# Kernel tuning notes

Measured on AMD Instinct MI355X. Metric: run time of the kernel, lower is better.

## Reference

```python
import jax, jax.numpy as jnp
import numpy as np

N_NODES = 100000
N_EDGES = 3200000
IN_FEATS = 512
HIDDEN = 16
NUM_CLASSES = 40


def setup_inputs() -> dict:
    key = jax.random.key(0)
    k1, k2, k3, k4, k5, k6 = jax.random.split(key, 6)
    x = jax.random.normal(k1, (N_NODES, IN_FEATS), dtype=jnp.float32)
    edge_index = jax.random.randint(k2, (2, N_EDGES), 0, N_NODES, dtype=jnp.int64)
    # Glorot-ish init for GCN weights
    W1 = jax.random.normal(k3, (IN_FEATS, HIDDEN), dtype=jnp.float32) / np.sqrt(IN_FEATS)
    b1 = jnp.zeros((HIDDEN,), dtype=jnp.float32)
    W2 = jax.random.normal(k4, (HIDDEN, NUM_CLASSES), dtype=jnp.float32) / np.sqrt(HIDDEN)
    b2 = jnp.zeros((NUM_CLASSES,), dtype=jnp.float32)
    return {"x": x, "edge_index": edge_index, "W1": W1, "b1": b1, "W2": W2, "b2": b2}


def _gcn_norm(edge_index, num_nodes):
    # Add self-loops (PyG GCNConv default), then symmetric normalization
    loops = jnp.arange(num_nodes, dtype=edge_index.dtype)
    src = jnp.concatenate([edge_index[0], loops])
    dst = jnp.concatenate([edge_index[1], loops])
    deg = jax.ops.segment_sum(jnp.ones_like(dst, dtype=jnp.float32), dst,
                              num_segments=num_nodes)
    dinv = jnp.where(deg > 0, jax.lax.rsqrt(deg), 0.0)
    norm = dinv[src] * dinv[dst]  # [E + N]
    return src, dst, norm


def _gcn_conv(x, W, b, src, dst, norm, num_nodes):
    h = x @ W                                   # transform first: [N, d_out]
    msg = h[src] * norm[:, None]                # gather + scale: [E+N, d_out]
    agg = jax.ops.segment_sum(msg, dst, num_segments=num_nodes)
    return agg + b


def reference(x, edge_index, W1, b1, W2, b2):
    num_nodes = x.shape[0]
    src, dst, norm = _gcn_norm(edge_index, num_nodes)
    h = _gcn_conv(x, W1, b1, src, dst, norm, num_nodes)
    h = jax.nn.relu(h)
    # F.dropout(training=self.training): eval mode -> identity (deterministic reference)
    h = _gcn_conv(h, W2, b2, src, dst, norm, num_nodes)
    return jax.nn.log_softmax(h, axis=1)
```

## Files before the change

### kernel.cpp

```cpp
#include <hip/hip_runtime.h>
#include <hip/hip_bf16.h>
#include <math.h>

#define N_NODES 100000
#define N_EDGES 3200000
#define IN_F    512
#define HID     16
#define NCLS    40
#define NB      2048
#define NPB     49
#define CAPW    2048
#define NBLK    256
#define EPB     12500

typedef unsigned short ushort_t;

__device__ __forceinline__ float bf16_to_f32(ushort_t u) {
    unsigned int b = ((unsigned int)u) << 16;
    return __uint_as_float(b);
}
__device__ __forceinline__ ushort_t f32_to_bf16(float f) {
    __hip_bfloat16 h = __float2bfloat16(f);
    return *(ushort_t*)&h;
}

__device__ __forceinline__ int load_edge(const void* ei, int is64, int idx) {
    if (is64) return (int)((const long long*)ei)[idx];
    return ((const int*)ei)[idx];
}

__global__ __launch_bounds__(256) void kPre(const int* __restrict__ ei,
                                            int* __restrict__ flag,
                                            int* __restrict__ gcur) {
    int i = blockIdx.x * 256 + threadIdx.x;
    if (i < NB) gcur[i] = i * CAPW;
    if (blockIdx.x == 0) {
        __shared__ int s_nz;
        if (threadIdx.x == 0) s_nz = 0;
        __syncthreads();
        int nz = 0;
        for (int k = threadIdx.x; k < 1024; k += 256)
            if (ei[2 * k + 1] != 0) nz = 1;
        if (nz) atomicOr(&s_nz, 1);
        __syncthreads();
        if (threadIdx.x == 0) flag[0] = s_nz ? 0 : 1;
    }
}

__global__ __launch_bounds__(256) void kB(const void* __restrict__ ei,
                                          const int* __restrict__ flag,
                                          int* __restrict__ gcur,
                                          int* __restrict__ binned) {
    __shared__ int hist[NB];
    __shared__ int base[NB];
    for (int i = threadIdx.x; i < NB; i += 256) hist[i] = 0;
    __syncthreads();
    int is64 = flag[0];
    int off0 = blockIdx.x * EPB;
    for (int i = threadIdx.x; i < EPB; i += 256) {
        int d = load_edge(ei, is64, N_EDGES + off0 + i);
        atomicAdd(&hist[d / NPB], 1);
    }
    __syncthreads();
    for (int i = threadIdx.x; i < NB; i += 256) {
        int c = hist[i];
        base[i] = c ? atomicAdd(&gcur[i], c) : 0;
        hist[i] = 0;
    }
    __syncthreads();
    for (int i = threadIdx.x; i < EPB; i += 256) {
        int s = load_edge(ei, is64, off0 + i);
        int d = load_edge(ei, is64, N_EDGES + off0 + i);
        int b = d / NPB;
        int o = atomicAdd(&hist[b], 1);
        binned[base[b] + o] = (s << 6) | (d - b * NPB);
    }
}

__global__ __launch_bounds__(256) void kSort(const int* __restrict__ gcur,
                                             int* __restrict__ binned,
                                             int* __restrict__ nstart,
                                             int* __restrict__ bend,
                                             float* __restrict__ dinv) {
    __shared__ int elist[CAPW];
    __shared__ int ih[NPB];
    __shared__ int lscan[NPB + 1];
    int b = blockIdx.x, tid = threadIdx.x;
    int beg = b * CAPW;
    int cnt = gcur[b] - beg;
    if (cnt > CAPW) cnt = CAPW;
    if (cnt < 0) cnt = 0;
    if (tid < NPB) ih[tid] = 0;
    __syncthreads();
    for (int k = tid; k < cnt; k += 256) {
        int p = binned[beg + k];
        elist[k] = p;
        atomicAdd(&ih[p & 63], 1);
    }
    __syncthreads();
    if (tid == 0) {
        int run = 0;
        for (int i = 0; i < NPB; ++i) { lscan[i] = run; run += ih[i]; }
        lscan[NPB] = run;
        bend[b] = beg + run;
    }
    __syncthreads();
    if (tid < NPB) {
        int n = b * NPB + tid;
        if (n < N_NODES) dinv[n] = rsqrtf((float)(ih[tid] + 1));
        nstart[n] = beg + lscan[tid];
        ih[tid] = lscan[tid];
    }
    __syncthreads();
    for (int k = tid; k < cnt; k += 256) {
        int p = elist[k];
        int pos = atomicAdd(&ih[p & 63], 1);
        binned[beg + pos] = p >> 6;
    }
}

__global__ __launch_bounds__(128) void k_gemm1(const float* __restrict__ x,
                                               const float* __restrict__ W1,
                                               const float* __restrict__ dinv,
                                               ushort_t* __restrict__ hsb) {
    __shared__ float Ws[IN_F * HID];
    for (int i = threadIdx.x; i < IN_F * HID; i += 128) Ws[i] = W1[i];
    __syncthreads();
    int n = blockIdx.x * 128 + threadIdx.x;
    if (n >= N_NODES) return;
    float acc[HID];
#pragma unroll
    for (int j = 0; j < HID; ++j) acc[j] = 0.0f;
    const float4* xr = (const float4*)(x + (size_t)n * IN_F);
    for (int k4 = 0; k4 < IN_F / 4; ++k4) {
        float4 xv = xr[k4];
        int kb = k4 * 4;
#pragma unroll
        for (int i = 0; i < 4; ++i) {
            float xs = (&xv.x)[i];
            const float4* wr = (const float4*)(Ws + (kb + i) * HID);
#pragma unroll
            for (int j4 = 0; j4 < 4; ++j4) {
                float4 w = wr[j4];
                acc[j4 * 4 + 0] += xs * w.x;
                acc[j4 * 4 + 1] += xs * w.y;
                acc[j4 * 4 + 2] += xs * w.z;
                acc[j4 * 4 + 3] += xs * w.w;
            }
        }
    }
    float di = dinv[n];
    ushort_t* hn = hsb + (size_t)n * HID;
#pragma unroll
    for (int j = 0; j < HID; ++j) hn[j] = f32_to_bf16(acc[j] * di);
}

__global__ __launch_bounds__(256) void kAgg1(const int* __restrict__ nstart,
                                             const int* __restrict__ bend,
                                             const int* __restrict__ sorted,
                                             const ushort_t* __restrict__ hsb,
                                             const float* __restrict__ dinv,
                                             const float* __restrict__ b1,
                                             ushort_t* __restrict__ h1sb) {
    int tid = threadIdx.x;
    int g = tid >> 4, lane = tid & 15;
    int n = blockIdx.x * 16 + g;
    int b = n / NPB, il = n - b * NPB;
    int beg = nstart[n];
    int end = (il == NPB - 1) ? bend[b] : nstart[n + 1];
    float acc = 0.0f;
    int k = beg;
    for (; k + 4 <= end; k += 4) {
        int s0 = sorted[k + 0], s1 = sorted[k + 1];
        int s2 = sorted[k + 2], s3 = sorted[k + 3];
        float v0 = bf16_to_f32(hsb[(size_t)s0 * HID + lane]);
        float v1 = bf16_to_f32(hsb[(size_t)s1 * HID + lane]);
        float v2 = bf16_to_f32(hsb[(size_t)s2 * HID + lane]);
        float v3 = bf16_to_f32(hsb[(size_t)s3 * HID + lane]);
        acc += (v0 + v1) + (v2 + v3);
    }
    for (; k < end; ++k)
        acc += bf16_to_f32(hsb[(size_t)sorted[k] * HID + lane]);
    float di = dinv[n];
    float self = bf16_to_f32(hsb[(size_t)n * HID + lane]);
    float v = di * (acc + self) + b1[lane];
    h1sb[(size_t)n * HID + lane] = f32_to_bf16(fmaxf(v, 0.0f) * di);
}

__global__ __launch_bounds__(256) void kAggOut(const int* __restrict__ nstart,
                                               const int* __restrict__ bend,
                                               const int* __restrict__ sorted,
                                               const ushort_t* __restrict__ h1sb,
                                               const float* __restrict__ dinv,
                                               const float* __restrict__ W2,
                                               const float* __restrict__ b2,
                                               float* __restrict__ out) {
    __shared__ float a2[16][HID + 1];
    __shared__ float Ws[HID * NCLS];
    __shared__ float bs[NCLS];
    int tid = threadIdx.x;
    for (int i = tid; i < HID * NCLS; i += 256) Ws[i] = W2[i];
    for (int i = tid; i < NCLS; i += 256) bs[i] = b2[i];

    int g = tid >> 4, lane = tid & 15;
    int n = blockIdx.x * 16 + g;
    int b = n / NPB, il = n - b * NPB;
    int beg = nstart[n];
    int end = (il == NPB - 1) ? bend[b] : nstart[n + 1];
    float acc = 0.0f;
    int k = beg;
    for (; k + 4 <= end; k += 4) {
        int s0 = sorted[k + 0], s1 = sorted[k + 1];
        int s2 = sorted[k + 2], s3 = sorted[k + 3];
        float v0 = bf16_to_f32(h1sb[(size_t)s0 * HID + lane]);
        float v1 = bf16_to_f32(h1sb[(size_t)s1 * HID + lane]);
        float v2 = bf16_to_f32(h1sb[(size_t)s2 * HID + lane]);
        float v3 = bf16_to_f32(h1sb[(size_t)s3 * HID + lane]);
        acc += (v0 + v1) + (v2 + v3);
    }
    for (; k < end; ++k)
        acc += bf16_to_f32(h1sb[(size_t)sorted[k] * HID + lane]);
    float di = dinv[n];
    float self = bf16_to_f32(h1sb[(size_t)n * HID + lane]);
    a2[g][lane] = di * (acc + self);
    __syncthreads();

    int v = g;
    int cidx = lane;
    float av[HID];
#pragma unroll
    for (int j = 0; j < HID; ++j) av[j] = a2[v][j];
    float l0 = bs[cidx], l1 = bs[cidx + 16];
    float l2 = (cidx < 8) ? bs[cidx + 32] : -1e30f;
#pragma unroll
    for (int j = 0; j < HID; ++j) {
        const float* wr = Ws + j * NCLS;
        l0 += av[j] * wr[cidx];
        l1 += av[j] * wr[cidx + 16];
        if (cidx < 8) l2 += av[j] * wr[cidx + 32];
    }
    float m = fmaxf(l0, fmaxf(l1, l2));
#pragma unroll
    for (int off = 8; off >= 1; off >>= 1)
        m = fmaxf(m, __shfl_xor(m, off, 16));
    float e = expf(l0 - m) + expf(l1 - m) + ((cidx < 8) ? expf(l2 - m) : 0.0f);
#pragma unroll
    for (int off = 8; off >= 1; off >>= 1)
        e += __shfl_xor(e, off, 16);
    float lse = m + logf(e);
    int nn = blockIdx.x * 16 + v;
    float* on = out + (size_t)nn * NCLS;
    on[cidx] = l0 - lse;
    on[cidx + 16] = l1 - lse;
    if (cidx < 8) on[cidx + 32] = l2 - lse;
}

extern "C" void kernel_launch(void* const* d_in, const int* in_sizes, int n_in,
                              void* d_out, int out_size, void* d_ws, size_t ws_size,
                              hipStream_t stream) {
    const float* x  = (const float*)d_in[0];
    const void*  ei = d_in[1];
    const float* W1 = (const float*)d_in[2];
    const float* b1 = (const float*)d_in[3];
    const float* W2 = (const float*)d_in[4];
    const float* b2 = (const float*)d_in[5];
    float* out = (float*)d_out;

    int*      iws    = (int*)d_ws;
    float*    fws    = (float*)d_ws;
    int*      gcur   = iws;
    int*      bend   = iws + 2048;
    int*      flag   = iws + 4096;
    float*    dinv   = fws + 8192;
    int*      nstart = iws + 108192;
    ushort_t* hsb    = (ushort_t*)(iws + 212992);
    ushort_t* h1sb   = (ushort_t*)(iws + 1012992);
    int*      binned = iws + 1812992;

    const int B = 256;

    kPre<<<(NB + B - 1) / B, B, 0, stream>>>((const int*)ei, flag, gcur);
    kB<<<NBLK, B, 0, stream>>>(ei, flag, gcur, binned);
    kSort<<<NB, B, 0, stream>>>(gcur, binned, nstart, bend, dinv);
    k_gemm1<<<(N_NODES + 127) / 128, 128, 0, stream>>>(x, W1, dinv, hsb);
    kAgg1<<<N_NODES / 16, B, 0, stream>>>(nstart, bend, binned, hsb, dinv, b1, h1sb);
    kAggOut<<<N_NODES / 16, B, 0, stream>>>(nstart, bend, binned, h1sb, dinv, W2, b2, out);
}
```

Measured before the change: 239.3 us.

## Run GEMM1 concurrently with edge binning in one kernel, defer dinv scaling

Merges the dense x@W1 projection and the edge-binning pass into one launch, with blocks split by index between the two roles, so the bandwidth-heavy GEMM overlaps with the atomic-heavy binning. Because dinv is not known yet when the GEMM runs, the GEMM writes unscaled bf16 rows and kSort rescales them by dinv after computing degrees. This adds a second bf16 rounding and an extra read-modify-write of hsb. GEMM blocks now use 256 threads instead of 128, with the same 32 KB of shared memory per block.

```diff
diff --git a/kernel.cpp b/kernel.cpp
--- a/kernel.cpp
+++ b/kernel.cpp
@@ -12,6 +12,7 @@
 #define CAPW    2048
 #define NBLK    256
 #define EPB     12500
+#define GEMM_BLKS 391
 
 typedef unsigned short ushort_t;
 
@@ -47,33 +48,70 @@
     }
 }
 
-__global__ __launch_bounds__(256) void kB(const void* __restrict__ ei,
-                                          const int* __restrict__ flag,
-                                          int* __restrict__ gcur,
-                                          int* __restrict__ binned) {
-    __shared__ int hist[NB];
-    __shared__ int base[NB];
-    for (int i = threadIdx.x; i < NB; i += 256) hist[i] = 0;
-    __syncthreads();
-    int is64 = flag[0];
-    int off0 = blockIdx.x * EPB;
-    for (int i = threadIdx.x; i < EPB; i += 256) {
-        int d = load_edge(ei, is64, N_EDGES + off0 + i);
-        atomicAdd(&hist[d / NPB], 1);
-    }
-    __syncthreads();
-    for (int i = threadIdx.x; i < NB; i += 256) {
-        int c = hist[i];
-        base[i] = c ? atomicAdd(&gcur[i], c) : 0;
-        hist[i] = 0;
-    }
-    __syncthreads();
-    for (int i = threadIdx.x; i < EPB; i += 256) {
-        int s = load_edge(ei, is64, off0 + i);
-        int d = load_edge(ei, is64, N_EDGES + off0 + i);
-        int b = d / NPB;
-        int o = atomicAdd(&hist[b], 1);
-        binned[base[b] + o] = (s << 6) | (d - b * NPB);
+__global__ __launch_bounds__(256) void kMega(const float* __restrict__ x,
+                                             const float* __restrict__ W1,
+                                             ushort_t* __restrict__ hsb,
+                                             const void* __restrict__ ei,
+                                             const int* __restrict__ flag,
+                                             int* __restrict__ gcur,
+                                             int* __restrict__ binned) {
+    __shared__ __align__(16) char smraw[IN_F * HID * 4];
+    int tid = threadIdx.x;
+    if (blockIdx.x < GEMM_BLKS) {
+        float* Ws = (float*)smraw;
+        for (int i = tid; i < IN_F * HID; i += 256) Ws[i] = W1[i];
+        __syncthreads();
+        int n = blockIdx.x * 256 + tid;
+        if (n >= N_NODES) return;
+        float acc[HID];
+#pragma unroll
+        for (int j = 0; j < HID; ++j) acc[j] = 0.0f;
+        const float4* xr = (const float4*)(x + (size_t)n * IN_F);
+        for (int k4 = 0; k4 < IN_F / 4; ++k4) {
+            float4 xv = xr[k4];
+            int kb = k4 * 4;
+#pragma unroll
+            for (int i = 0; i < 4; ++i) {
+                float xs = (&xv.x)[i];
+                const float4* wr = (const float4*)(Ws + (kb + i) * HID);
+#pragma unroll
+                for (int j4 = 0; j4 < 4; ++j4) {
+                    float4 w = wr[j4];
+                    acc[j4 * 4 + 0] += xs * w.x;
+                    acc[j4 * 4 + 1] += xs * w.y;
+                    acc[j4 * 4 + 2] += xs * w.z;
+                    acc[j4 * 4 + 3] += xs * w.w;
+                }
+            }
+        }
+        ushort_t* hn = hsb + (size_t)n * HID;
+#pragma unroll
+        for (int j = 0; j < HID; ++j) hn[j] = f32_to_bf16(acc[j]);
+    } else {
+        int* hist = (int*)smraw;
+        int* base = (int*)(smraw + NB * 4);
+        for (int i = tid; i < NB; i += 256) hist[i] = 0;
+        __syncthreads();
+        int is64 = flag[0];
+        int off0 = (blockIdx.x - GEMM_BLKS) * EPB;
+        for (int i = tid; i < EPB; i += 256) {
+            int d = load_edge(ei, is64, N_EDGES + off0 + i);
+            atomicAdd(&hist[d / NPB], 1);
+        }
+        __syncthreads();
+        for (int i = tid; i < NB; i += 256) {
+            int c = hist[i];
+            base[i] = c ? atomicAdd(&gcur[i], c) : 0;
+            hist[i] = 0;
+        }
+        __syncthreads();
+        for (int i = tid; i < EPB; i += 256) {
+            int s = load_edge(ei, is64, off0 + i);
+            int d = load_edge(ei, is64, N_EDGES + off0 + i);
+            int b = d / NPB;
+            int o = atomicAdd(&hist[b], 1);
+            binned[base[b] + o] = (s << 6) | (d - b * NPB);
+        }
     }
 }
 
@@ -81,10 +119,12 @@
                                              int* __restrict__ binned,
                                              int* __restrict__ nstart,
                                              int* __restrict__ bend,
-                                             float* __restrict__ dinv) {
+                                             float* __restrict__ dinv,
+                                             ushort_t* __restrict__ hsb) {
     __shared__ int elist[CAPW];
     __shared__ int ih[NPB];
     __shared__ int lscan[NPB + 1];
+    __shared__ float sdinv[NPB];
     int b = blockIdx.x, tid = threadIdx.x;
     int beg = b * CAPW;
     int cnt = gcur[b] - beg;
@@ -107,7 +147,9 @@
     __syncthreads();
     if (tid < NPB) {
         int n = b * NPB + tid;
-        if (n < N_NODES) dinv[n] = rsqrtf((float)(ih[tid] + 1));
+        float di = rsqrtf((float)(ih[tid] + 1));
+        sdinv[tid] = di;
+        if (n < N_NODES) dinv[n] = di;
         nstart[n] = beg + lscan[tid];
         ih[tid] = lscan[tid];
     }
@@ -117,42 +159,14 @@
         int pos = atomicAdd(&ih[p & 63], 1);
         binned[beg + pos] = p >> 6;
     }
-}
-
-__global__ __launch_bounds__(128) void k_gemm1(const float* __restrict__ x,
-                                               const float* __restrict__ W1,
-                                               const float* __restrict__ dinv,
-                                               ushort_t* __restrict__ hsb) {
-    __shared__ float Ws[IN_F * HID];
-    for (int i = threadIdx.x; i < IN_F * HID; i += 128) Ws[i] = W1[i];
-    __syncthreads();
-    int n = blockIdx.x * 128 + threadIdx.x;
-    if (n >= N_NODES) return;
-    float acc[HID];
-#pragma unroll
-    for (int j = 0; j < HID; ++j) acc[j] = 0.0f;
-    const float4* xr = (const float4*)(x + (size_t)n * IN_F);
-    for (int k4 = 0; k4 < IN_F / 4; ++k4) {
-        float4 xv = xr[k4];
-        int kb = k4 * 4;
-#pragma unroll
-        for (int i = 0; i < 4; ++i) {
-            float xs = (&xv.x)[i];
-            const float4* wr = (const float4*)(Ws + (kb + i) * HID);
-#pragma unroll
-            for (int j4 = 0; j4 < 4; ++j4) {
-                float4 w = wr[j4];
-                acc[j4 * 4 + 0] += xs * w.x;
-                acc[j4 * 4 + 1] += xs * w.y;
-                acc[j4 * 4 + 2] += xs * w.z;
-                acc[j4 * 4 + 3] += xs * w.w;
-            }
-        }
-    }
-    float di = dinv[n];
-    ushort_t* hn = hsb + (size_t)n * HID;
-#pragma unroll
-    for (int j = 0; j < HID; ++j) hn[j] = f32_to_bf16(acc[j] * di);
+    for (int u = tid; u < NPB * HID; u += 256) {
+        int i = u >> 4, j = u & 15;
+        int n = b * NPB + i;
+        if (n < N_NODES) {
+            size_t idx = (size_t)n * HID + j;
+            hsb[idx] = f32_to_bf16(bf16_to_f32(hsb[idx]) * sdinv[i]);
+        }
+    }
 }
 
 __global__ __launch_bounds__(256) void kAgg1(const int* __restrict__ nstart,
@@ -225,8 +239,7 @@
     a2[g][lane] = di * (acc + self);
     __syncthreads();
 
-    int v = g;
-    int cidx = lane;
+    int v = g, cidx = lane;
     float av[HID];
 #pragma unroll
     for (int j = 0; j < HID; ++j) av[j] = a2[v][j];
@@ -280,9 +293,8 @@
     const int B = 256;
 
     kPre<<<(NB + B - 1) / B, B, 0, stream>>>((const int*)ei, flag, gcur);
-    kB<<<NBLK, B, 0, stream>>>(ei, flag, gcur, binned);
-    kSort<<<NB, B, 0, stream>>>(gcur, binned, nstart, bend, dinv);
-    k_gemm1<<<(N_NODES + 127) / 128, 128, 0, stream>>>(x, W1, dinv, hsb);
+    kMega<<<GEMM_BLKS + NBLK, B, 0, stream>>>(x, W1, hsb, ei, flag, gcur, binned);
+    kSort<<<NB, B, 0, stream>>>(gcur, binned, nstart, bend, dinv, hsb);
     kAgg1<<<N_NODES / 16, B, 0, stream>>>(nstart, bend, binned, hsb, dinv, b1, h1sb);
     kAggOut<<<N_NODES / 16, B, 0, stream>>>(nstart, bend, binned, h1sb, dinv, W2, b2, out);
 }
```

New measurement: 241.3 us. Within noise of the previous version (+0.9%).
